# Kernel optimization log

Measured on AMD Instinct MI355X. Metric: run time of the kernel, lower is better.

Reference implementation:

```python
import jax, jax.numpy as jnp
import numpy as np

N, E, D, H, L, G, OUT = 100000, 1600000, 64, 64, 3, 128, 10
BN_EPS = 1e-5

def setup_inputs() -> dict:
    key = jax.random.key(0)
    ks = jax.random.split(key, 8)
    x = jax.random.normal(ks[0], (N, D), dtype=jnp.float32)
    edge_index = jax.random.randint(ks[1], (2, E), 0, N, dtype=jnp.int64)
    batch = jnp.sort(jax.random.randint(ks[2], (N,), 0, G, dtype=jnp.int64))
    W1 = jax.random.normal(ks[3], (L, D, H), dtype=jnp.float32) / np.sqrt(D)
    b1 = jnp.zeros((L, H), dtype=jnp.float32)
    gamma = jnp.ones((L, H), dtype=jnp.float32)
    beta = jnp.zeros((L, H), dtype=jnp.float32)
    W2 = jax.random.normal(ks[4], (L, H, H), dtype=jnp.float32) / np.sqrt(H)
    b2 = jnp.zeros((L, H), dtype=jnp.float32)
    Wout = jax.random.normal(ks[5], (L, H, OUT), dtype=jnp.float32) / np.sqrt(H)
    bout = jnp.zeros((L, OUT), dtype=jnp.float32)
    return {"x": x, "edge_index": edge_index, "batch": batch, "W1": W1, "b1": b1,
            "gamma": gamma, "beta": beta, "W2": W2, "b2": b2, "Wout": Wout, "bout": bout}

def _gin_layer(x, src, dst, W1, b1, g, bt, W2, b2):
    # GIN sum aggregation, eps = 0: (1+eps)*x + sum_{j->i} x_j
    agg = x + jax.ops.segment_sum(x[src], dst, num_segments=x.shape[0])
    h = agg @ W1 + b1
    mu = jnp.mean(h, axis=0)
    var = jnp.var(h, axis=0)
    h = (h - mu) * jax.lax.rsqrt(var + BN_EPS) * g + bt  # BatchNorm1d (batch stats)
    h = jax.nn.relu(h)
    return h @ W2 + b2

def reference(x, edge_index, batch, W1, b1, gamma, beta, W2, b2, Wout, bout):
    src, dst = edge_index[0], edge_index[1]
    score = jnp.zeros((G, OUT), dtype=x.dtype)
    for l in range(L):
        x = _gin_layer(x, src, dst, W1[l], b1[l], gamma[l], beta[l], W2[l], b2[l])
        pooled = jax.ops.segment_sum(x, batch, num_segments=G)  # global_add_pool
        score = score + (pooled @ Wout[l] + bout[l])  # dropout is identity in eval
    return score
```

## Files before the change

kernel.cpp:

```cpp
#include <hip/hip_runtime.h>

typedef unsigned int uint;
typedef short bf16x8 __attribute__((ext_vector_type(8)));
typedef float f32x4 __attribute__((ext_vector_type(4)));

#define N_NODES 100000
#define E_EDGES 1600000
#define L_LAYERS 3
#define G_GRAPHS 128
#define OUT_F 10
#define BN_EPS 1e-5f

#define BSHIFT 7
#define NSTRIPE ((N_NODES + 127) >> 7)
#define CHUNK 2048
#define NCHUNK ((E_EDGES + CHUNK - 1) / CHUNK)
#define PAD8(d) (((d) + 7) & ~7)
#define BCAP (2048 * 103)
#define FB_GRID (103 * 8)
#define SCAP 2560
#define SNBR 3584

__device__ __forceinline__ uint bf_pack(float a, float b) {
    uint ua = __float_as_uint(a);
    ua = (ua + 0x7fffu + ((ua >> 16) & 1u)) >> 16;
    uint ub = __float_as_uint(b);
    ub = (ub + 0x7fffu + ((ub >> 16) & 1u)) >> 16;
    return ua | (ub << 16);
}
__device__ __forceinline__ unsigned short bf1(float a) {
    uint ua = __float_as_uint(a);
    return (unsigned short)((ua + 0x7fffu + ((ua >> 16) & 1u)) >> 16);
}
__device__ __forceinline__ float lo16(uint u) { return __uint_as_float(u << 16); }
__device__ __forceinline__ float hi16(uint u) { return __uint_as_float(u & 0xffff0000u); }

__global__ __launch_bounds__(256) void init_kernel(int* __restrict__ gcur,
                                                   int* __restrict__ scur) {
    int t = blockIdx.x * 256 + threadIdx.x;
    if (t < 8) gcur[t] = t * BCAP;
    if (t < NSTRIPE) scur[t] = t * SCAP;
}

__global__ __launch_bounds__(256) void fillA_kernel(
    const int* __restrict__ src, const int* __restrict__ dst,
    int* __restrict__ gcur, int2* __restrict__ epair) {
    __shared__ int lcnt[8];
    __shared__ int lbase[8];
    int tid = threadIdx.x;
    int base = blockIdx.x * CHUNK;
    if (tid < 8) lcnt[tid] = 0;
    __syncthreads();

    int sd[8], ss[8], bk[8], off[8];
    #pragma unroll
    for (int it = 0; it < 8; ++it) {
        int e = base + it * 256 + tid;
        bk[it] = -1;
        if (e < E_EDGES) {
            sd[it] = dst[e];
            ss[it] = src[e];
            bk[it] = (sd[it] >> BSHIFT) & 7;
            off[it] = atomicAdd(&lcnt[bk[it]], 1);
        }
    }
    __syncthreads();
    if (tid < 8) lbase[tid] = atomicAdd(&gcur[tid], lcnt[tid]);
    __syncthreads();
    #pragma unroll
    for (int it = 0; it < 8; ++it) {
        if (bk[it] >= 0)
            epair[lbase[bk[it]] + off[it]] = make_int2(ss[it], sd[it]);
    }
}

__global__ __launch_bounds__(256) void fillB2_kernel(
    const int2* __restrict__ epair1, const int* __restrict__ gcur,
    int* __restrict__ scur, int2* __restrict__ epair2) {
    __shared__ int lcnt[98];
    __shared__ int lbase[98];
    int tid = threadIdx.x;
    int g = blockIdx.x & 7;
    int c = blockIdx.x >> 3;
    int ebeg = g * BCAP + c * CHUNK;
    int eend = gcur[g];
    if (tid < 98) lcnt[tid] = 0;
    __syncthreads();

    int2 pp[8]; int bk[8], off[8];
    #pragma unroll
    for (int it = 0; it < 8; ++it) {
        int i = ebeg + it * 256 + tid;
        bk[it] = -1;
        if (i < eend) {
            pp[it] = epair1[i];
            bk[it] = pp[it].y >> 10;
            off[it] = atomicAdd(&lcnt[bk[it]], 1);
        }
    }
    __syncthreads();
    if (tid < 98 && lcnt[tid] > 0)
        lbase[tid] = atomicAdd(&scur[(tid << 3) | g], lcnt[tid]);
    __syncthreads();
    #pragma unroll
    for (int it = 0; it < 8; ++it) {
        if (bk[it] >= 0)
            epair2[lbase[bk[it]] + off[it]] = pp[it];
    }
}

__global__ __launch_bounds__(256) void fillC2_kernel(
    const int2* __restrict__ epair2, const int* __restrict__ scur,
    int* __restrict__ rbeg, int* __restrict__ rend, int* __restrict__ nbr) {
    __shared__ int cnt[128];
    __shared__ int loc[128];
    __shared__ int off[128];
    __shared__ int buf[SNBR];
    __shared__ int stotal;
    int s = blockIdx.x;
    int tid = threadIdx.x;
    int node0 = s << 7;
    int qbeg = s * SCAP;
    int qend = scur[s];
    if (tid < 128) cnt[tid] = 0;
    __syncthreads();

    for (int i = qbeg + tid; i < qend; i += 256)
        atomicAdd(&cnt[epair2[i].y & 127], 1);
    __syncthreads();

    int v = (tid < 128) ? PAD8(cnt[tid]) : 0;
    if (tid < 128) loc[tid] = v;
    __syncthreads();
    for (int o = 1; o < 128; o <<= 1) {
        int u = (tid < 128 && tid >= o) ? loc[tid - o] : 0;
        __syncthreads();
        if (tid < 128) loc[tid] += u;
        __syncthreads();
    }
    int sbase = s * SNBR;
    if (tid < 128) {
        int ex = loc[tid] - v;
        off[tid] = ex;
        int node = node0 + tid;
        if (node < N_NODES) {
            rbeg[node] = sbase + ex;
            rend[node] = sbase + ex + v;
        }
    }
    if (tid == 0) stotal = loc[127];
    __syncthreads();
    int total = stotal;

    for (int i = tid; i < total; i += 256) buf[i] = N_NODES;
    __syncthreads();

    for (int i = qbeg + tid; i < qend; i += 256) {
        int2 p = epair2[i];
        int pos = atomicAdd(&off[p.y & 127], 1);
        buf[pos] = p.x;
    }
    __syncthreads();

    for (int i = tid * 4; i < total; i += 1024)
        *reinterpret_cast<int4*>(nbr + sbase + i) = *reinterpret_cast<const int4*>(buf + i);
}

__global__ __launch_bounds__(256) void tobf_kernel(const float* __restrict__ x,
                                                   uint* __restrict__ xbf) {
    int i = blockIdx.x * 256 + threadIdx.x;
    if (i < N_NODES * 8) {
        float4 a = reinterpret_cast<const float4*>(x)[i * 2];
        float4 b = reinterpret_cast<const float4*>(x)[i * 2 + 1];
        uint4 o;
        o.x = bf_pack(a.x, a.y);
        o.y = bf_pack(a.z, a.w);
        o.z = bf_pack(b.x, b.y);
        o.w = bf_pack(b.z, b.w);
        reinterpret_cast<uint4*>(xbf)[i] = o;
    }
    if (i < 8) reinterpret_cast<uint4*>(xbf)[N_NODES * 8 + i] = make_uint4(0, 0, 0, 0);
}

__global__ __launch_bounds__(256) void gemm1_fused_kernel(
    const uint* __restrict__ xbf, const int* __restrict__ rbeg,
    const int* __restrict__ rend, const int* __restrict__ nbr,
    const float* __restrict__ W1, const float* __restrict__ b1,
    unsigned short* __restrict__ h16, float* __restrict__ stats) {
    __shared__ unsigned short sA[64][72];
    __shared__ unsigned short sW[64][72];
    int tid = threadIdx.x;
    int row0 = blockIdx.x * 64;

    for (int i = tid; i < 1024; i += 256) {
        int k = i >> 4, cb = (i & 15) * 4;
        float4 w = reinterpret_cast<const float4*>(W1)[i];
        sW[cb + 0][k] = bf1(w.x);
        sW[cb + 1][k] = bf1(w.y);
        sW[cb + 2][k] = bf1(w.z);
        sW[cb + 3][k] = bf1(w.w);
    }

    const uint4* xb4 = reinterpret_cast<const uint4*>(xbf);
    int c8 = tid & 7;
    int rslot = tid >> 3;
    for (int rr = 0; rr < 2; ++rr) {
        int r = rslot + 32 * rr;
        int gr = row0 + r;
        float a0 = 0.f, a1 = 0.f, a2 = 0.f, a3 = 0.f;
        float a4 = 0.f, a5 = 0.f, a6 = 0.f, a7 = 0.f;
        if (gr < N_NODES) {
            uint4 sv = xb4[(size_t)gr * 8 + c8];
            a0 = lo16(sv.x); a1 = hi16(sv.x); a2 = lo16(sv.y); a3 = hi16(sv.y);
            a4 = lo16(sv.z); a5 = hi16(sv.z); a6 = lo16(sv.w); a7 = hi16(sv.w);
            int beg = rbeg[gr], end = rend[gr];
            int4 ia = *reinterpret_cast<const int4*>(nbr + beg);
            int4 ib = *reinterpret_cast<const int4*>(nbr + beg + 4);
            for (int j = beg; j < end; j += 8) {
                int4 ian = *reinterpret_cast<const int4*>(nbr + j + 8);
                int4 ibn = *reinterpret_cast<const int4*>(nbr + j + 12);
                uint4 v0 = xb4[(size_t)ia.x * 8 + c8];
                uint4 v1 = xb4[(size_t)ia.y * 8 + c8];
                uint4 v2 = xb4[(size_t)ia.z * 8 + c8];
                uint4 v3 = xb4[(size_t)ia.w * 8 + c8];
                uint4 v4 = xb4[(size_t)ib.x * 8 + c8];
                uint4 v5 = xb4[(size_t)ib.y * 8 + c8];
                uint4 v6 = xb4[(size_t)ib.z * 8 + c8];
                uint4 v7 = xb4[(size_t)ib.w * 8 + c8];
                a0 += lo16(v0.x); a1 += hi16(v0.x); a2 += lo16(v0.y); a3 += hi16(v0.y);
                a4 += lo16(v0.z); a5 += hi16(v0.z); a6 += lo16(v0.w); a7 += hi16(v0.w);
                a0 += lo16(v1.x); a1 += hi16(v1.x); a2 += lo16(v1.y); a3 += hi16(v1.y);
                a4 += lo16(v1.z); a5 += hi16(v1.z); a6 += lo16(v1.w); a7 += hi16(v1.w);
                a0 += lo16(v2.x); a1 += hi16(v2.x); a2 += lo16(v2.y); a3 += hi16(v2.y);
                a4 += lo16(v2.z); a5 += hi16(v2.z); a6 += lo16(v2.w); a7 += hi16(v2.w);
                a0 += lo16(v3.x); a1 += hi16(v3.x); a2 += lo16(v3.y); a3 += hi16(v3.y);
                a4 += lo16(v3.z); a5 += hi16(v3.z); a6 += lo16(v3.w); a7 += hi16(v3.w);
                a0 += lo16(v4.x); a1 += hi16(v4.x); a2 += lo16(v4.y); a3 += hi16(v4.y);
                a4 += lo16(v4.z); a5 += hi16(v4.z); a6 += lo16(v4.w); a7 += hi16(v4.w);
                a0 += lo16(v5.x); a1 += hi16(v5.x); a2 += lo16(v5.y); a3 += hi16(v5.y);
                a4 += lo16(v5.z); a5 += hi16(v5.z); a6 += lo16(v5.w); a7 += hi16(v5.w);
                a0 += lo16(v6.x); a1 += hi16(v6.x); a2 += lo16(v6.y); a3 += hi16(v6.y);
                a4 += lo16(v6.z); a5 += hi16(v6.z); a6 += lo16(v6.w); a7 += hi16(v6.w);
                a0 += lo16(v7.x); a1 += hi16(v7.x); a2 += lo16(v7.y); a3 += hi16(v7.y);
                a4 += lo16(v7.z); a5 += hi16(v7.z); a6 += lo16(v7.w); a7 += hi16(v7.w);
                ia = ian; ib = ibn;
            }
        }
        uint4 o;
        o.x = bf_pack(a0, a1); o.y = bf_pack(a2, a3);
        o.z = bf_pack(a4, a5); o.w = bf_pack(a6, a7);
        *reinterpret_cast<uint4*>(&sA[r][c8 * 8]) = o;
    }
    __syncthreads();

    int w = tid >> 6;
    int l = tid & 63;
    int lr = l & 15;
    int lk = l >> 4;
    f32x4 acc[4];
    #pragma unroll
    for (int ct = 0; ct < 4; ++ct) {
        float b = b1[ct * 16 + lr];
        acc[ct] = (f32x4){b, b, b, b};
    }
    #pragma unroll
    for (int ct = 0; ct < 4; ++ct) {
        #pragma unroll
        for (int kc = 0; kc < 2; ++kc) {
            bf16x8 av = *reinterpret_cast<const bf16x8*>(&sA[w * 16 + lr][kc * 32 + lk * 8]);
            bf16x8 bv = *reinterpret_cast<const bf16x8*>(&sW[ct * 16 + lr][kc * 32 + lk * 8]);
            acc[ct] = __builtin_amdgcn_mfma_f32_16x16x32_bf16(av, bv, acc[ct], 0, 0, 0);
        }
    }

    float s4[4] = {0.f, 0.f, 0.f, 0.f};
    float q4[4] = {0.f, 0.f, 0.f, 0.f};
    #pragma unroll
    for (int ct = 0; ct < 4; ++ct) {
        #pragma unroll
        for (int r = 0; r < 4; ++r) {
            int row = row0 + w * 16 + lk * 4 + r;
            float v = acc[ct][r];
            if (row < N_NODES) {
                h16[(size_t)row * 64 + ct * 16 + lr] = bf1(v);
                s4[ct] += v;
                q4[ct] += v * v;
            }
        }
    }
    __syncthreads();
    float* scr = reinterpret_cast<float*>(&sW[0][0]);
    int g16 = w * 4 + lk;
    #pragma unroll
    for (int ct = 0; ct < 4; ++ct) {
        scr[g16 * 64 + ct * 16 + lr] = s4[ct];
        scr[1024 + g16 * 64 + ct * 16 + lr] = q4[ct];
    }
    __syncthreads();
    if (tid < 64) {
        float s = 0.f, q = 0.f;
        #pragma unroll
        for (int r2 = 0; r2 < 16; ++r2) {
            s += scr[r2 * 64 + tid];
            q += scr[1024 + r2 * 64 + tid];
        }
        unsafeAtomicAdd(&stats[tid], s);
        unsafeAtomicAdd(&stats[64 + tid], q);
    }
}

__global__ __launch_bounds__(256) void gemm2_pool_kernel(
    const unsigned short* __restrict__ h16, const float* __restrict__ stats,
    const float* __restrict__ gamma, const float* __restrict__ beta,
    const float* __restrict__ W2, const float* __restrict__ b2,
    const int* __restrict__ batch, float* __restrict__ pooled,
    unsigned short* __restrict__ xout) {
    __shared__ unsigned short sA[64][72];
    __shared__ unsigned short sW[64][72];
    int tid = threadIdx.x;
    int row0 = blockIdx.x * 64;

    for (int i = tid; i < 1024; i += 256) {
        int k = i >> 4, cb = (i & 15) * 4;
        float4 w = reinterpret_cast<const float4*>(W2)[i];
        sW[cb + 0][k] = bf1(w.x);
        sW[cb + 1][k] = bf1(w.y);
        sW[cb + 2][k] = bf1(w.z);
        sW[cb + 3][k] = bf1(w.w);
    }

    int c8 = tid & 7;
    float scv[8], shv[8];
    #pragma unroll
    for (int k = 0; k < 8; ++k) {
        int col = c8 * 8 + k;
        float mu = stats[col] * (1.0f / N_NODES);
        float var = stats[64 + col] * (1.0f / N_NODES) - mu * mu;
        scv[k] = gamma[col] * rsqrtf(var + BN_EPS);
        shv[k] = beta[col] - mu * scv[k];
    }

    const uint4* h4 = reinterpret_cast<const uint4*>(h16);
    for (int i = tid; i < 512; i += 256) {
        int r = i >> 3;
        int gr = row0 + r;
        float o[8] = {0.f, 0.f, 0.f, 0.f, 0.f, 0.f, 0.f, 0.f};
        if (gr < N_NODES) {
            uint4 v = h4[(size_t)gr * 8 + c8];
            float f[8] = {lo16(v.x), hi16(v.x), lo16(v.y), hi16(v.y),
                          lo16(v.z), hi16(v.z), lo16(v.w), hi16(v.w)};
            #pragma unroll
            for (int k = 0; k < 8; ++k)
                o[k] = fmaxf(fmaf(f[k], scv[k], shv[k]), 0.f);
        }
        uint4 p;
        p.x = bf_pack(o[0], o[1]); p.y = bf_pack(o[2], o[3]);
        p.z = bf_pack(o[4], o[5]); p.w = bf_pack(o[6], o[7]);
        *reinterpret_cast<uint4*>(&sA[r][c8 * 8]) = p;
    }
    __syncthreads();

    int w = tid >> 6;
    int l = tid & 63;
    int lr = l & 15;
    int lk = l >> 4;
    f32x4 acc[4];
    #pragma unroll
    for (int ct = 0; ct < 4; ++ct) {
        float b = b2[ct * 16 + lr];
        acc[ct] = (f32x4){b, b, b, b};
    }
    #pragma unroll
    for (int ct = 0; ct < 4; ++ct) {
        #pragma unroll
        for (int kc = 0; kc < 2; ++kc) {
            bf16x8 av = *reinterpret_cast<const bf16x8*>(&sA[w * 16 + lr][kc * 32 + lk * 8]);
            bf16x8 bv = *reinterpret_cast<const bf16x8*>(&sW[ct * 16 + lr][kc * 32 + lk * 8]);
            acc[ct] = __builtin_amdgcn_mfma_f32_16x16x32_bf16(av, bv, acc[ct], 0, 0, 0);
        }
    }

    #pragma unroll
    for (int ct = 0; ct < 4; ++ct) {
        #pragma unroll
        for (int r = 0; r < 4; ++r) {
            int row = row0 + w * 16 + lk * 4 + r;
            if (row < N_NODES)
                xout[(size_t)row * 64 + ct * 16 + lr] = bf1(acc[ct][r]);
        }
    }

    int lastrow = row0 + 63; if (lastrow >= N_NODES) lastrow = N_NODES - 1;
    int b0 = batch[row0], bL = batch[lastrow];
    if (b0 == bL) {
        float ps[4] = {0.f, 0.f, 0.f, 0.f};
        #pragma unroll
        for (int ct = 0; ct < 4; ++ct) {
            #pragma unroll
            for (int r = 0; r < 4; ++r) {
                int row = row0 + w * 16 + lk * 4 + r;
                if (row < N_NODES) ps[ct] += acc[ct][r];
            }
        }
        __syncthreads();
        float* scr = reinterpret_cast<float*>(&sW[0][0]);
        int g16 = w * 4 + lk;
        #pragma unroll
        for (int ct = 0; ct < 4; ++ct)
            scr[g16 * 64 + ct * 16 + lr] = ps[ct];
        __syncthreads();
        if (tid < 64) {
            float s = 0.f;
            #pragma unroll
            for (int r2 = 0; r2 < 16; ++r2) s += scr[r2 * 64 + tid];
            unsafeAtomicAdd(&pooled[b0 * 64 + tid], s);
        }
    } else {
        #pragma unroll
        for (int ct = 0; ct < 4; ++ct) {
            float pacc = 0.f;
            int curb = -1;
            int col = ct * 16 + lr;
            #pragma unroll
            for (int r = 0; r < 4; ++r) {
                int row = row0 + w * 16 + lk * 4 + r;
                if (row < N_NODES) {
                    int b = batch[row];
                    if (b != curb) {
                        if (curb >= 0) unsafeAtomicAdd(&pooled[curb * 64 + col], pacc);
                        curb = b;
                        pacc = 0.f;
                    }
                    pacc += acc[ct][r];
                }
            }
            if (curb >= 0) unsafeAtomicAdd(&pooled[curb * 64 + col], pacc);
        }
    }
}

__global__ void out_kernel(const float* __restrict__ pooled,
                           const float* __restrict__ Wout,
                           const float* __restrict__ bout,
                           float* __restrict__ score) {
    int idx = blockIdx.x * blockDim.x + threadIdx.x;
    if (idx >= G_GRAPHS * OUT_F) return;
    int g = idx / OUT_F;
    int o = idx - g * OUT_F;
    float acc = bout[o];
    #pragma unroll
    for (int k = 0; k < 64; ++k) acc += pooled[g * 64 + k] * Wout[k * OUT_F + o];
    score[idx] += acc;
}

extern "C" void kernel_launch(void* const* d_in, const int* in_sizes, int n_in,
                              void* d_out, int out_size, void* d_ws, size_t ws_size,
                              hipStream_t stream) {
    const float* x     = (const float*)d_in[0];
    const int*   ei    = (const int*)d_in[1];
    const int*   batch = (const int*)d_in[2];
    const float* W1    = (const float*)d_in[3];
    const float* b1    = (const float*)d_in[4];
    const float* gamma = (const float*)d_in[5];
    const float* beta  = (const float*)d_in[6];
    const float* W2    = (const float*)d_in[7];
    const float* b2    = (const float*)d_in[8];
    const float* Wout  = (const float*)d_in[9];
    const float* bout  = (const float*)d_in[10];
    float* out = (float*)d_out;

    unsigned short* H16 = (unsigned short*)d_ws;
    uint*  XBF    = (uint*)(H16 + (size_t)N_NODES * 64);
    float* stats  = (float*)(XBF + (size_t)(N_NODES + 1) * 32);
    float* pooled = stats + 128;
    int*   gcur   = (int*)(pooled + (size_t)G_GRAPHS * 64);
    int*   scur   = gcur + 8;
    int*   rbeg   = scur + 784;
    int*   rend   = rbeg + N_NODES;
    int*   nbr    = rend + N_NODES;
    int2*  epair1 = (int2*)(nbr + (size_t)NSTRIPE * SNBR + 16);
    int2*  epair2 = epair1 + (size_t)8 * BCAP;

    const int* src = ei;
    const int* dst = ei + E_EDGES;

    (void)hipMemsetAsync(d_out, 0, (size_t)G_GRAPHS * OUT_F * sizeof(float), stream);

    init_kernel<<<(NSTRIPE + 255) / 256, 256, 0, stream>>>(gcur, scur);
    fillA_kernel<<<NCHUNK, 256, 0, stream>>>(src, dst, gcur, epair1);
    fillB2_kernel<<<FB_GRID, 256, 0, stream>>>(epair1, gcur, scur, epair2);
    fillC2_kernel<<<NSTRIPE, 256, 0, stream>>>(epair2, scur, rbeg, rend, nbr);
    tobf_kernel<<<(N_NODES * 8 + 255) / 256, 256, 0, stream>>>(x, XBF);

    int nb = (N_NODES + 63) / 64;

    for (int l = 0; l < L_LAYERS; ++l) {
        (void)hipMemsetAsync(stats, 0, (128 + (size_t)G_GRAPHS * 64) * sizeof(float), stream);

        gemm1_fused_kernel<<<nb, 256, 0, stream>>>(XBF, rbeg, rend, nbr,
            W1 + l * 64 * 64, b1 + l * 64, H16, stats);
        gemm2_pool_kernel<<<nb, 256, 0, stream>>>(H16, stats,
            gamma + l * 64, beta + l * 64, W2 + l * 64 * 64, b2 + l * 64, batch,
            pooled, (unsigned short*)XBF);
        out_kernel<<<(G_GRAPHS * OUT_F + 127) / 128, 128, 0, stream>>>(
            pooled, Wout + l * 64 * OUT_F, bout + l * OUT_F, out);
    }
}
```

Baseline: 316.3 us.

## Interleave two-row neighbor gathers and batch per-layer output and memsets

Result: slower. 331.1 us, median of 2 (+4.7%).

```diff
diff --git a/kernel.cpp b/kernel.cpp
--- a/kernel.cpp
+++ b/kernel.cpp
@@ -36,9 +36,11 @@
 __device__ __forceinline__ float hi16(uint u) { return __uint_as_float(u & 0xffff0000u); }
 
 __global__ __launch_bounds__(256) void init_kernel(int* __restrict__ gcur,
-                                                   int* __restrict__ scur) {
+                                                   int* __restrict__ scur,
+                                                   int* __restrict__ sent) {
     int t = blockIdx.x * 256 + threadIdx.x;
     if (t < 8) gcur[t] = t * BCAP;
+    if (t < 16) sent[t] = N_NODES;
     if (t < NSTRIPE) scur[t] = t * SCAP;
 }
 
@@ -182,9 +184,14 @@
     if (i < 8) reinterpret_cast<uint4*>(xbf)[N_NODES * 8 + i] = make_uint4(0, 0, 0, 0);
 }
 
+#define ACC8(vv, t0, t1, t2, t3, t4, t5, t6, t7) \
+    t0 += lo16(vv.x); t1 += hi16(vv.x); t2 += lo16(vv.y); t3 += hi16(vv.y); \
+    t4 += lo16(vv.z); t5 += hi16(vv.z); t6 += lo16(vv.w); t7 += hi16(vv.w);
+
 __global__ __launch_bounds__(256) void gemm1_fused_kernel(
     const uint* __restrict__ xbf, const int* __restrict__ rbeg,
     const int* __restrict__ rend, const int* __restrict__ nbr,
+    const int* __restrict__ sent,
     const float* __restrict__ W1, const float* __restrict__ b1,
     unsigned short* __restrict__ h16, float* __restrict__ stats) {
     __shared__ unsigned short sA[64][72];
@@ -204,52 +211,75 @@
     const uint4* xb4 = reinterpret_cast<const uint4*>(xbf);
     int c8 = tid & 7;
     int rslot = tid >> 3;
-    for (int rr = 0; rr < 2; ++rr) {
-        int r = rslot + 32 * rr;
-        int gr = row0 + r;
-        float a0 = 0.f, a1 = 0.f, a2 = 0.f, a3 = 0.f;
-        float a4 = 0.f, a5 = 0.f, a6 = 0.f, a7 = 0.f;
-        if (gr < N_NODES) {
-            uint4 sv = xb4[(size_t)gr * 8 + c8];
-            a0 = lo16(sv.x); a1 = hi16(sv.x); a2 = lo16(sv.y); a3 = hi16(sv.y);
-            a4 = lo16(sv.z); a5 = hi16(sv.z); a6 = lo16(sv.w); a7 = hi16(sv.w);
-            int beg = rbeg[gr], end = rend[gr];
-            int4 ia = *reinterpret_cast<const int4*>(nbr + beg);
-            int4 ib = *reinterpret_cast<const int4*>(nbr + beg + 4);
-            for (int j = beg; j < end; j += 8) {
-                int4 ian = *reinterpret_cast<const int4*>(nbr + j + 8);
-                int4 ibn = *reinterpret_cast<const int4*>(nbr + j + 12);
-                uint4 v0 = xb4[(size_t)ia.x * 8 + c8];
-                uint4 v1 = xb4[(size_t)ia.y * 8 + c8];
-                uint4 v2 = xb4[(size_t)ia.z * 8 + c8];
-                uint4 v3 = xb4[(size_t)ia.w * 8 + c8];
-                uint4 v4 = xb4[(size_t)ib.x * 8 + c8];
-                uint4 v5 = xb4[(size_t)ib.y * 8 + c8];
-                uint4 v6 = xb4[(size_t)ib.z * 8 + c8];
-                uint4 v7 = xb4[(size_t)ib.w * 8 + c8];
-                a0 += lo16(v0.x); a1 += hi16(v0.x); a2 += lo16(v0.y); a3 += hi16(v0.y);
-                a4 += lo16(v0.z); a5 += hi16(v0.z); a6 += lo16(v0.w); a7 += hi16(v0.w);
-                a0 += lo16(v1.x); a1 += hi16(v1.x); a2 += lo16(v1.y); a3 += hi16(v1.y);
-                a4 += lo16(v1.z); a5 += hi16(v1.z); a6 += lo16(v1.w); a7 += hi16(v1.w);
-                a0 += lo16(v2.x); a1 += hi16(v2.x); a2 += lo16(v2.y); a3 += hi16(v2.y);
-                a4 += lo16(v2.z); a5 += hi16(v2.z); a6 += lo16(v2.w); a7 += hi16(v2.w);
-                a0 += lo16(v3.x); a1 += hi16(v3.x); a2 += lo16(v3.y); a3 += hi16(v3.y);
-                a4 += lo16(v3.z); a5 += hi16(v3.z); a6 += lo16(v3.w); a7 += hi16(v3.w);
-                a0 += lo16(v4.x); a1 += hi16(v4.x); a2 += lo16(v4.y); a3 += hi16(v4.y);
-                a4 += lo16(v4.z); a5 += hi16(v4.z); a6 += lo16(v4.w); a7 += hi16(v4.w);
-                a0 += lo16(v5.x); a1 += hi16(v5.x); a2 += lo16(v5.y); a3 += hi16(v5.y);
-                a4 += lo16(v5.z); a5 += hi16(v5.z); a6 += lo16(v5.w); a7 += hi16(v5.w);
-                a0 += lo16(v6.x); a1 += hi16(v6.x); a2 += lo16(v6.y); a3 += hi16(v6.y);
-                a4 += lo16(v6.z); a5 += hi16(v6.z); a6 += lo16(v6.w); a7 += hi16(v6.w);
-                a0 += lo16(v7.x); a1 += hi16(v7.x); a2 += lo16(v7.y); a3 += hi16(v7.y);
-                a4 += lo16(v7.z); a5 += hi16(v7.z); a6 += lo16(v7.w); a7 += hi16(v7.w);
-                ia = ian; ib = ibn;
-            }
-        }
-        uint4 o;
-        o.x = bf_pack(a0, a1); o.y = bf_pack(a2, a3);
-        o.z = bf_pack(a4, a5); o.w = bf_pack(a6, a7);
-        *reinterpret_cast<uint4*>(&sA[r][c8 * 8]) = o;
+    int gr1 = row0 + rslot;
+    int gr2 = row0 + rslot + 32;
+    bool val1 = gr1 < N_NODES, val2 = gr2 < N_NODES;
+
+    float a0 = 0.f, a1 = 0.f, a2 = 0.f, a3 = 0.f;
+    float a4 = 0.f, a5 = 0.f, a6 = 0.f, a7 = 0.f;
+    float d0 = 0.f, d1 = 0.f, d2 = 0.f, d3 = 0.f;
+    float d4 = 0.f, d5 = 0.f, d6 = 0.f, d7 = 0.f;
+    if (val1) {
+        uint4 sv = xb4[(size_t)gr1 * 8 + c8];
+        ACC8(sv, a0, a1, a2, a3, a4, a5, a6, a7)
+    }
+    if (val2) {
+        uint4 sv = xb4[(size_t)gr2 * 8 + c8];
+        ACC8(sv, d0, d1, d2, d3, d4, d5, d6, d7)
+    }
+    int beg1 = val1 ? rbeg[gr1] : 0, end1 = val1 ? rend[gr1] : 0;
+    int beg2 = val2 ? rbeg[gr2] : 0, end2 = val2 ? rend[gr2] : 0;
+    int len1 = end1 - beg1, len2 = end2 - beg2;
+    int nmax = len1 > len2 ? len1 : len2;
+    for (int o = 0; o < nmax; o += 8) {
+        const int* p1 = (o < len1) ? (nbr + beg1 + o) : sent;
+        const int* p2 = (o < len2) ? (nbr + beg2 + o) : sent;
+        int4 ia1 = *reinterpret_cast<const int4*>(p1);
+        int4 ib1 = *reinterpret_cast<const int4*>(p1 + 4);
+        int4 ia2 = *reinterpret_cast<const int4*>(p2);
+        int4 ib2 = *reinterpret_cast<const int4*>(p2 + 4);
+        uint4 u0 = xb4[(size_t)ia1.x * 8 + c8];
+        uint4 u1 = xb4[(size_t)ia1.y * 8 + c8];
+        uint4 u2 = xb4[(size_t)ia1.z * 8 + c8];
+        uint4 u3 = xb4[(size_t)ia1.w * 8 + c8];
+        uint4 u4 = xb4[(size_t)ib1.x * 8 + c8];
+        uint4 u5 = xb4[(size_t)ib1.y * 8 + c8];
+        uint4 u6 = xb4[(size_t)ib1.z * 8 + c8];
+        uint4 u7 = xb4[(size_t)ib1.w * 8 + c8];
+        uint4 w0 = xb4[(size_t)ia2.x * 8 + c8];
+        uint4 w1 = xb4[(size_t)ia2.y * 8 + c8];
+        uint4 w2 = xb4[(size_t)ia2.z * 8 + c8];
+        uint4 w3 = xb4[(size_t)ia2.w * 8 + c8];
+        uint4 w4 = xb4[(size_t)ib2.x * 8 + c8];
+        uint4 w5 = xb4[(size_t)ib2.y * 8 + c8];
+        uint4 w6 = xb4[(size_t)ib2.z * 8 + c8];
+        uint4 w7 = xb4[(size_t)ib2.w * 8 + c8];
+        ACC8(u0, a0, a1, a2, a3, a4, a5, a6, a7)
+        ACC8(u1, a0, a1, a2, a3, a4, a5, a6, a7)
+        ACC8(u2, a0, a1, a2, a3, a4, a5, a6, a7)
+        ACC8(u3, a0, a1, a2, a3, a4, a5, a6, a7)
+        ACC8(u4, a0, a1, a2, a3, a4, a5, a6, a7)
+        ACC8(u5, a0, a1, a2, a3, a4, a5, a6, a7)
+        ACC8(u6, a0, a1, a2, a3, a4, a5, a6, a7)
+        ACC8(u7, a0, a1, a2, a3, a4, a5, a6, a7)
+        ACC8(w0, d0, d1, d2, d3, d4, d5, d6, d7)
+        ACC8(w1, d0, d1, d2, d3, d4, d5, d6, d7)
+        ACC8(w2, d0, d1, d2, d3, d4, d5, d6, d7)
+        ACC8(w3, d0, d1, d2, d3, d4, d5, d6, d7)
+        ACC8(w4, d0, d1, d2, d3, d4, d5, d6, d7)
+        ACC8(w5, d0, d1, d2, d3, d4, d5, d6, d7)
+        ACC8(w6, d0, d1, d2, d3, d4, d5, d6, d7)
+        ACC8(w7, d0, d1, d2, d3, d4, d5, d6, d7)
+    }
+    {
+        uint4 o1;
+        o1.x = bf_pack(a0, a1); o1.y = bf_pack(a2, a3);
+        o1.z = bf_pack(a4, a5); o1.w = bf_pack(a6, a7);
+        *reinterpret_cast<uint4*>(&sA[rslot][c8 * 8]) = o1;
+        uint4 o2;
+        o2.x = bf_pack(d0, d1); o2.y = bf_pack(d2, d3);
+        o2.z = bf_pack(d4, d5); o2.w = bf_pack(d6, d7);
+        *reinterpret_cast<uint4*>(&sA[rslot + 32][c8 * 8]) = o2;
     }
     __syncthreads();
 
@@ -380,18 +410,21 @@
         }
     }
 
-    #pragma unroll
-    for (int ct = 0; ct < 4; ++ct) {
-        #pragma unroll
-        for (int r = 0; r < 4; ++r) {
-            int row = row0 + w * 16 + lk * 4 + r;
-            if (row < N_NODES)
-                xout[(size_t)row * 64 + ct * 16 + lr] = bf1(acc[ct][r]);
+    if (xout) {
+        #pragma unroll
+        for (int ct = 0; ct < 4; ++ct) {
+            #pragma unroll
+            for (int r = 0; r < 4; ++r) {
+                int row = row0 + w * 16 + lk * 4 + r;
+                if (row < N_NODES)
+                    xout[(size_t)row * 64 + ct * 16 + lr] = bf1(acc[ct][r]);
+            }
         }
     }
 
     int lastrow = row0 + 63; if (lastrow >= N_NODES) lastrow = N_NODES - 1;
-    int b0 = batch[row0], bL = batch[lastrow];
+    int b0 = batch[row0 < N_NODES ? row0 : N_NODES - 1], bL = batch[lastrow];
+    int g16 = w * 4 + lk;
     if (b0 == bL) {
         float ps[4] = {0.f, 0.f, 0.f, 0.f};
         #pragma unroll
@@ -404,7 +437,6 @@
         }
         __syncthreads();
         float* scr = reinterpret_cast<float*>(&sW[0][0]);
-        int g16 = w * 4 + lk;
         #pragma unroll
         for (int ct = 0; ct < 4; ++ct)
             scr[g16 * 64 + ct * 16 + lr] = ps[ct];
@@ -439,18 +471,23 @@
     }
 }
 
-__global__ void out_kernel(const float* __restrict__ pooled,
-                           const float* __restrict__ Wout,
-                           const float* __restrict__ bout,
-                           float* __restrict__ score) {
+__global__ void out3_kernel(const float* __restrict__ pooled3,
+                            const float* __restrict__ Wout,
+                            const float* __restrict__ bout,
+                            float* __restrict__ score) {
     int idx = blockIdx.x * blockDim.x + threadIdx.x;
     if (idx >= G_GRAPHS * OUT_F) return;
     int g = idx / OUT_F;
     int o = idx - g * OUT_F;
-    float acc = bout[o];
-    #pragma unroll
-    for (int k = 0; k < 64; ++k) acc += pooled[g * 64 + k] * Wout[k * OUT_F + o];
-    score[idx] += acc;
+    float acc = 0.f;
+    for (int l = 0; l < L_LAYERS; ++l) {
+        acc += bout[l * OUT_F + o];
+        const float* pl = pooled3 + (size_t)l * G_GRAPHS * 64 + g * 64;
+        const float* wl = Wout + l * 64 * OUT_F;
+        #pragma unroll
+        for (int k = 0; k < 64; ++k) acc += pl[k] * wl[k * OUT_F + o];
+    }
+    score[idx] = acc;
 }
 
 extern "C" void kernel_launch(void* const* d_in, const int* in_sizes, int n_in,
@@ -471,10 +508,11 @@
 
     unsigned short* H16 = (unsigned short*)d_ws;
     uint*  XBF    = (uint*)(H16 + (size_t)N_NODES * 64);
-    float* stats  = (float*)(XBF + (size_t)(N_NODES + 1) * 32);
-    float* pooled = stats + 128;
-    int*   gcur   = (int*)(pooled + (size_t)G_GRAPHS * 64);
-    int*   scur   = gcur + 8;
+    float* stats3 = (float*)(XBF + (size_t)(N_NODES + 1) * 32);
+    float* pooled3= stats3 + 3 * 128;
+    int*   gcur   = (int*)(pooled3 + (size_t)3 * G_GRAPHS * 64);
+    int*   sent   = gcur + 8;
+    int*   scur   = sent + 16;
     int*   rbeg   = scur + 784;
     int*   rend   = rbeg + N_NODES;
     int*   nbr    = rend + N_NODES;
@@ -484,9 +522,9 @@
     const int* src = ei;
     const int* dst = ei + E_EDGES;
 
-    (void)hipMemsetAsync(d_out, 0, (size_t)G_GRAPHS * OUT_F * sizeof(float), stream);
-
-    init_kernel<<<(NSTRIPE + 255) / 256, 256, 0, stream>>>(gcur, scur);
+    (void)hipMemsetAsync(stats3, 0, (3 * 128 + (size_t)3 * G_GRAPHS * 64) * sizeof(float), stream);
+
+    init_kernel<<<(NSTRIPE + 255) / 256, 256, 0, stream>>>(gcur, scur, sent);
     fillA_kernel<<<NCHUNK, 256, 0, stream>>>(src, dst, gcur, epair1);
     fillB2_kernel<<<FB_GRID, 256, 0, stream>>>(epair1, gcur, scur, epair2);
     fillC2_kernel<<<NSTRIPE, 256, 0, stream>>>(epair2, scur, rbeg, rend, nbr);
@@ -495,14 +533,16 @@
     int nb = (N_NODES + 63) / 64;
 
     for (int l = 0; l < L_LAYERS; ++l) {
-        (void)hipMemsetAsync(stats, 0, (128 + (size_t)G_GRAPHS * 64) * sizeof(float), stream);
-
-        gemm1_fused_kernel<<<nb, 256, 0, stream>>>(XBF, rbeg, rend, nbr,
+        float* stats = stats3 + l * 128;
+        float* pooled = pooled3 + (size_t)l * G_GRAPHS * 64;
+        gemm1_fused_kernel<<<nb, 256, 0, stream>>>(XBF, rbeg, rend, nbr, sent,
             W1 + l * 64 * 64, b1 + l * 64, H16, stats);
+        unsigned short* xout = (l == L_LAYERS - 1) ? (unsigned short*)nullptr
+                                                   : (unsigned short*)XBF;
         gemm2_pool_kernel<<<nb, 256, 0, stream>>>(H16, stats,
             gamma + l * 64, beta + l * 64, W2 + l * 64 * 64, b2 + l * 64, batch,
-            pooled, (unsigned short*)XBF);
-        out_kernel<<<(G_GRAPHS * OUT_F + 127) / 128, 128, 0, stream>>>(
-            pooled, Wout + l * 64 * OUT_F, bout + l * OUT_F, out);
-    }
-}
+            pooled, xout);
+    }
+    out3_kernel<<<(G_GRAPHS * OUT_F + 127) / 128, 128, 0, stream>>>(
+        pooled3, Wout, bout, out);
+}
```
